# Kernel tuning notes

Hardware: AMD Instinct MI355X
Metric: run time of the kernel (lower is better)

Reference implementation:

```python
import jax, jax.numpy as jnp
import numpy as np

B = 192
D = 2048   # input_size
H = 128
LOG2PI = float(np.log(2.0 * np.pi))


def _linear_params(key, fan_in, fan_out):
    k1, k2 = jax.random.split(key)
    s = 1.0 / np.sqrt(fan_in)
    w = jax.random.uniform(k1, (fan_out, fan_in), minval=-s, maxval=s, dtype=jnp.float32)
    b = jax.random.uniform(k2, (fan_out,), minval=-s, maxval=s, dtype=jnp.float32)
    return w, b


def setup_inputs() -> dict:
    key = jax.random.key(0)
    ks = jax.random.split(key, 8)
    q = jax.random.normal(ks[0], (B, D), dtype=jnp.float32)
    eps = jax.random.normal(ks[1], (B, B, D), dtype=jnp.float32)  # rsample noise
    mu_w1, mu_b1 = _linear_params(ks[2], D, H)
    mu_w2, mu_b2 = _linear_params(ks[3], H, H)
    mu_w3, mu_b3 = _linear_params(ks[4], H, D)
    lv_w1, lv_b1 = _linear_params(ks[5], D, H)
    lv_w2, lv_b2 = _linear_params(ks[6], H, H)
    lv_w3, lv_b3 = _linear_params(ks[7], H, D)
    return dict(q=q, eps=eps,
                mu_w1=mu_w1, mu_b1=mu_b1, mu_w2=mu_w2, mu_b2=mu_b2, mu_w3=mu_w3, mu_b3=mu_b3,
                lv_w1=lv_w1, lv_b1=lv_b1, lv_w2=lv_w2, lv_b2=lv_b2, lv_w3=lv_w3, lv_b3=lv_b3)


def reference(q, eps, mu_w1, mu_b1, mu_w2, mu_b2, mu_w3, mu_b3,
              lv_w1, lv_b1, lv_w2, lv_b2, lv_w3, lv_b3):
    relu = jax.nn.relu
    # mu head (ReLU on every layer, including the last, as in the torch code)
    mu = relu(q @ mu_w1.T + mu_b1)
    mu = relu(mu @ mu_w2.T + mu_b2)
    mu = relu(mu @ mu_w3.T + mu_b3)                    # [B, D]
    # logvar head
    lv = relu(q @ lv_w1.T + lv_b1)
    lv = relu(lv @ lv_w2.T + lv_b2)
    lv = relu(lv @ lv_w3.T + lv_b3)                    # [B, D]
    # torch passes std_mat = diag(exp(0.5*logvar)) as COVARIANCE matrix,
    # so the diagonal variance is var = exp(0.5*logvar), per-dim scale = sqrt(var).
    var = jnp.exp(0.5 * lv)                            # [B, D] covariance diagonal
    scale = jnp.sqrt(var)                              # = exp(0.25*logvar)
    # rsample with sample_shape=(B,): p[i, j] = mu[j] + scale[j] * eps[i, j]
    p = mu[None, :, :] + eps * scale[None, :, :]       # [B, B, D]
    # diagonal-Gaussian log_prob of distribution j evaluated at p[i, j]
    diff = p - mu[None, :, :]
    maha = jnp.sum(diff * diff / var[None, :, :], axis=-1)       # [B, B]
    logdet = 0.5 * jnp.sum(lv, axis=-1)                          # sum(log var) = 0.5*sum(logvar)
    log_prob = -0.5 * (maha + D * LOG2PI) - 0.5 * logdet[None, :]  # [B, B]
    return p, log_prob
```

## Files before the change

kernel.cpp:

```cpp
#include <hip/hip_runtime.h>
#include <math.h>

#define BB 192
#define DD 2048
#define HH 128

#define D_LOG2PI 3763.9722320063395f

typedef float f32x4 __attribute__((ext_vector_type(4)));

__global__ __launch_bounds__(256) void head_kernel(
    const float* __restrict__ q,
    const float* __restrict__ mw1, const float* __restrict__ mb1,
    const float* __restrict__ mw2, const float* __restrict__ mb2,
    const float* __restrict__ mw3, const float* __restrict__ mb3,
    const float* __restrict__ lw1, const float* __restrict__ lb1,
    const float* __restrict__ lw2, const float* __restrict__ lb2,
    const float* __restrict__ lw3, const float* __restrict__ lb3,
    float* __restrict__ mu_out, float* __restrict__ scale_out,
    float* __restrict__ invvar_out, float* __restrict__ logdet_out)
{
    const int row  = blockIdx.x;
    const int head = blockIdx.y;
    const float* W1 = head ? lw1 : mw1;
    const float* B1 = head ? lb1 : mb1;
    const float* W2 = head ? lw2 : mw2;
    const float* B2 = head ? lb2 : mb2;
    const float* W3 = head ? lw3 : mw3;
    const float* B3 = head ? lb3 : mb3;

    __shared__ float qrow[DD];
    __shared__ float h1[HH];
    __shared__ float h2[HH];
    __shared__ float red[4];

    const int t = threadIdx.x;

    {
        const f32x4* src = (const f32x4*)(q + (size_t)row * DD);
        f32x4* dst = (f32x4*)qrow;
        for (int i = t; i < DD / 4; i += 256) dst[i] = src[i];
    }
    __syncthreads();

    {
        const int o = t >> 1, half = t & 1;
        const f32x4* w4 = (const f32x4*)(W1 + (size_t)o * DD + half * (DD / 2));
        const f32x4* x4 = (const f32x4*)(qrow + half * (DD / 2));
        float acc = 0.f;
        #pragma unroll 4
        for (int k = 0; k < DD / 8; ++k) {
            f32x4 w = w4[k], x = x4[k];
            acc += w.x * x.x + w.y * x.y + w.z * x.z + w.w * x.w;
        }
        acc += __shfl_xor(acc, 1);
        if (half == 0) h1[o] = fmaxf(acc + B1[o], 0.f);
    }
    __syncthreads();

    {
        const int o = t >> 1, half = t & 1;
        const f32x4* w4 = (const f32x4*)(W2 + o * HH + half * (HH / 2));
        const f32x4* x4 = (const f32x4*)(h1 + half * (HH / 2));
        float acc = 0.f;
        #pragma unroll
        for (int k = 0; k < HH / 8; ++k) {
            f32x4 w = w4[k], x = x4[k];
            acc += w.x * x.x + w.y * x.y + w.z * x.z + w.w * x.w;
        }
        acc += __shfl_xor(acc, 1);
        if (half == 0) h2[o] = fmaxf(acc + B2[o], 0.f);
    }
    __syncthreads();

    float sumlv = 0.f;
    for (int m = 0; m < DD / 256; ++m) {
        const int j = m * 256 + t;
        const f32x4* w4 = (const f32x4*)(W3 + (size_t)j * HH);
        const f32x4* x4 = (const f32x4*)h2;
        float acc = 0.f;
        #pragma unroll
        for (int k = 0; k < HH / 4; ++k) {
            f32x4 w = w4[k], x = x4[k];
            acc += w.x * x.x + w.y * x.y + w.z * x.z + w.w * x.w;
        }
        float val = fmaxf(acc + B3[j], 0.f);
        if (head == 0) {
            mu_out[(size_t)row * DD + j] = val;
        } else {
            float var = expf(0.5f * val);
            float sc  = sqrtf(var);
            scale_out [(size_t)row * DD + j] = sc;
            invvar_out[(size_t)row * DD + j] = 1.0f / var;
            sumlv += val;
        }
    }
    if (head == 1) {
        #pragma unroll
        for (int off = 32; off; off >>= 1) sumlv += __shfl_down(sumlv, off);
        const int wid = t >> 6, lane = t & 63;
        if (lane == 0) red[wid] = sumlv;
        __syncthreads();
        if (t == 0) logdet_out[row] = 0.5f * (red[0] + red[1] + red[2] + red[3]);
    }
}

__global__ __launch_bounds__(256) void sample_logprob_kernel(
    const float* __restrict__ eps,
    const float* __restrict__ mu, const float* __restrict__ scale,
    const float* __restrict__ invvar, const float* __restrict__ logdet,
    float* __restrict__ p_out, float* __restrict__ lp_out)
{
    const int i = blockIdx.x;
    const int j = blockIdx.y;
    const int t = threadIdx.x;

    const size_t base = ((size_t)(i * BB + j)) * DD;
    const f32x4* e4  = (const f32x4*)(eps + base);
    const f32x4* m4  = (const f32x4*)(mu + (size_t)j * DD);
    const f32x4* s4  = (const f32x4*)(scale + (size_t)j * DD);
    const f32x4* iv4 = (const f32x4*)(invvar + (size_t)j * DD);
    f32x4* p4 = (f32x4*)(p_out + base);

    float acc = 0.f;
    #pragma unroll
    for (int it = 0; it < DD / 1024; ++it) {
        const int idx = it * 256 + t;
        f32x4 e  = __builtin_nontemporal_load(&e4[idx]);
        f32x4 m  = m4[idx];
        f32x4 s  = s4[idx];
        f32x4 iv = iv4[idx];
        f32x4 pv;
        pv.x = m.x + e.x * s.x;
        pv.y = m.y + e.y * s.y;
        pv.z = m.z + e.z * s.z;
        pv.w = m.w + e.w * s.w;
        float dx = pv.x - m.x, dy = pv.y - m.y, dz = pv.z - m.z, dw = pv.w - m.w;
        acc += dx * dx * iv.x;
        acc += dy * dy * iv.y;
        acc += dz * dz * iv.z;
        acc += dw * dw * iv.w;
        __builtin_nontemporal_store(pv, &p4[idx]);
    }

    #pragma unroll
    for (int off = 32; off; off >>= 1) acc += __shfl_down(acc, off);
    __shared__ float red[4];
    const int wid = t >> 6, lane = t & 63;
    if (lane == 0) red[wid] = acc;
    __syncthreads();
    if (t == 0) {
        const float maha = red[0] + red[1] + red[2] + red[3];
        lp_out[(size_t)i * BB + j] = -0.5f * (maha + D_LOG2PI) - 0.5f * logdet[j];
    }
}

extern "C" void kernel_launch(void* const* d_in, const int* in_sizes, int n_in,
                              void* d_out, int out_size, void* d_ws, size_t ws_size,
                              hipStream_t stream) {
    (void)in_sizes; (void)n_in; (void)out_size; (void)ws_size;
    const float* q    = (const float*)d_in[0];
    const float* eps  = (const float*)d_in[1];
    const float* mw1  = (const float*)d_in[2];
    const float* mb1  = (const float*)d_in[3];
    const float* mw2  = (const float*)d_in[4];
    const float* mb2  = (const float*)d_in[5];
    const float* mw3  = (const float*)d_in[6];
    const float* mb3  = (const float*)d_in[7];
    const float* lw1  = (const float*)d_in[8];
    const float* lb1  = (const float*)d_in[9];
    const float* lw2  = (const float*)d_in[10];
    const float* lb2  = (const float*)d_in[11];
    const float* lw3  = (const float*)d_in[12];
    const float* lb3  = (const float*)d_in[13];

    float* ws      = (float*)d_ws;
    float* mu      = ws;
    float* scale   = ws + (size_t)BB * DD;
    float* invvar  = ws + 2 * (size_t)BB * DD;
    float* logdet  = ws + 3 * (size_t)BB * DD;

    float* p  = (float*)d_out;
    float* lp = p + (size_t)BB * BB * DD;

    head_kernel<<<dim3(BB, 2), 256, 0, stream>>>(
        q, mw1, mb1, mw2, mb2, mw3, mb3, lw1, lb1, lw2, lb2, lw3, lb3,
        mu, scale, invvar, logdet);

    sample_logprob_kernel<<<dim3(BB, BB), 256, 0, stream>>>(
        eps, mu, scale, invvar, logdet, p, lp);
}
```

Baseline: 656.2 us.

## Process two rows per head block with coalesced wave-level dot products; single-wave sample blocks

The head kernel now handles two batch rows per 512-thread block and reuses each weight load for both rows. Each layer is restructured so a wave (or half-wave) reads a weight row in a coalesced way and reduces with shuffles. The sample/log-prob kernel switches to 64-thread blocks, which removes the shared-memory reduction and block barrier. The intent is to halve weight traffic in the heads and cut per-block sync overhead in the bandwidth-bound sample kernel, at the cost of fewer, larger head blocks and more serial work per sample thread.

```diff
diff --git a/kernel.cpp b/kernel.cpp
--- a/kernel.cpp
+++ b/kernel.cpp
@@ -9,7 +9,7 @@
 
 typedef float f32x4 __attribute__((ext_vector_type(4)));
 
-__global__ __launch_bounds__(256) void head_kernel(
+__global__ __launch_bounds__(512) void head_kernel(
     const float* __restrict__ q,
     const float* __restrict__ mw1, const float* __restrict__ mb1,
     const float* __restrict__ mw2, const float* __restrict__ mb2,
@@ -20,7 +20,7 @@
     float* __restrict__ mu_out, float* __restrict__ scale_out,
     float* __restrict__ invvar_out, float* __restrict__ logdet_out)
 {
-    const int row  = blockIdx.x;
+    const int row0 = blockIdx.x * 2;
     const int head = blockIdx.y;
     const float* W1 = head ? lw1 : mw1;
     const float* B1 = head ? lb1 : mb1;
@@ -29,83 +29,138 @@
     const float* W3 = head ? lw3 : mw3;
     const float* B3 = head ? lb3 : mb3;
 
-    __shared__ float qrow[DD];
-    __shared__ float h1[HH];
-    __shared__ float h2[HH];
-    __shared__ float red[4];
-
-    const int t = threadIdx.x;
-
-    {
-        const f32x4* src = (const f32x4*)(q + (size_t)row * DD);
+    __shared__ float qrow[2 * DD];
+    __shared__ float h1[2][HH];
+    __shared__ float h2[2][HH];
+    __shared__ float red[8][2];
+
+    const int t    = threadIdx.x;
+    const int wave = t >> 6;
+    const int lane = t & 63;
+    const int half = lane >> 5;
+    const int kl   = lane & 31;
+
+    {
+        const f32x4* src = (const f32x4*)(q + (size_t)row0 * DD);
         f32x4* dst = (f32x4*)qrow;
-        for (int i = t; i < DD / 4; i += 256) dst[i] = src[i];
+        #pragma unroll
+        for (int it = 0; it < (2 * DD / 4) / 512; ++it)
+            dst[it * 512 + t] = src[it * 512 + t];
     }
     __syncthreads();
 
     {
-        const int o = t >> 1, half = t & 1;
-        const f32x4* w4 = (const f32x4*)(W1 + (size_t)o * DD + half * (DD / 2));
-        const f32x4* x4 = (const f32x4*)(qrow + half * (DD / 2));
-        float acc = 0.f;
-        #pragma unroll 4
-        for (int k = 0; k < DD / 8; ++k) {
-            f32x4 w = w4[k], x = x4[k];
-            acc += w.x * x.x + w.y * x.y + w.z * x.z + w.w * x.w;
-        }
-        acc += __shfl_xor(acc, 1);
-        if (half == 0) h1[o] = fmaxf(acc + B1[o], 0.f);
+        const f32x4* q0 = (const f32x4*)qrow;
+        const f32x4* q1 = (const f32x4*)(qrow + DD);
+        for (int oi = 0; oi < 16; ++oi) {
+            const int o = wave * 16 + oi;
+            const f32x4* w4 = (const f32x4*)(W1 + (size_t)o * DD);
+            float a0 = 0.f, a1 = 0.f;
+            #pragma unroll
+            for (int k = 0; k < DD / 4 / 64; ++k) {
+                f32x4 w  = w4[k * 64 + lane];
+                f32x4 x0 = q0[k * 64 + lane];
+                f32x4 x1 = q1[k * 64 + lane];
+                a0 += w.x * x0.x + w.y * x0.y + w.z * x0.z + w.w * x0.w;
+                a1 += w.x * x1.x + w.y * x1.y + w.z * x1.z + w.w * x1.w;
+            }
+            #pragma unroll
+            for (int off = 32; off; off >>= 1) {
+                a0 += __shfl_xor(a0, off);
+                a1 += __shfl_xor(a1, off);
+            }
+            if (lane == 0) {
+                const float b = B1[o];
+                h1[0][o] = fmaxf(a0 + b, 0.f);
+                h1[1][o] = fmaxf(a1 + b, 0.f);
+            }
+        }
     }
     __syncthreads();
 
     {
-        const int o = t >> 1, half = t & 1;
-        const f32x4* w4 = (const f32x4*)(W2 + o * HH + half * (HH / 2));
-        const f32x4* x4 = (const f32x4*)(h1 + half * (HH / 2));
-        float acc = 0.f;
+        const f32x4* x0 = (const f32x4*)h1[0];
+        const f32x4* x1 = (const f32x4*)h1[1];
         #pragma unroll
-        for (int k = 0; k < HH / 8; ++k) {
-            f32x4 w = w4[k], x = x4[k];
-            acc += w.x * x.x + w.y * x.y + w.z * x.z + w.w * x.w;
-        }
-        acc += __shfl_xor(acc, 1);
-        if (half == 0) h2[o] = fmaxf(acc + B2[o], 0.f);
+        for (int pi = 0; pi < 8; ++pi) {
+            const int o = wave * 16 + pi * 2 + half;
+            const f32x4* w4 = (const f32x4*)(W2 + (size_t)o * HH);
+            f32x4 w  = w4[kl];
+            f32x4 v0 = x0[kl];
+            f32x4 v1 = x1[kl];
+            float a0 = w.x * v0.x + w.y * v0.y + w.z * v0.z + w.w * v0.w;
+            float a1 = w.x * v1.x + w.y * v1.y + w.z * v1.z + w.w * v1.w;
+            #pragma unroll
+            for (int off = 16; off; off >>= 1) {
+                a0 += __shfl_xor(a0, off);
+                a1 += __shfl_xor(a1, off);
+            }
+            if (kl == 0) {
+                const float b = B2[o];
+                h2[0][o] = fmaxf(a0 + b, 0.f);
+                h2[1][o] = fmaxf(a1 + b, 0.f);
+            }
+        }
     }
     __syncthreads();
 
-    float sumlv = 0.f;
-    for (int m = 0; m < DD / 256; ++m) {
-        const int j = m * 256 + t;
-        const f32x4* w4 = (const f32x4*)(W3 + (size_t)j * HH);
-        const f32x4* x4 = (const f32x4*)h2;
-        float acc = 0.f;
-        #pragma unroll
-        for (int k = 0; k < HH / 4; ++k) {
-            f32x4 w = w4[k], x = x4[k];
-            acc += w.x * x.x + w.y * x.y + w.z * x.z + w.w * x.w;
-        }
-        float val = fmaxf(acc + B3[j], 0.f);
-        if (head == 0) {
-            mu_out[(size_t)row * DD + j] = val;
-        } else {
-            float var = expf(0.5f * val);
-            float sc  = sqrtf(var);
-            scale_out [(size_t)row * DD + j] = sc;
-            invvar_out[(size_t)row * DD + j] = 1.0f / var;
-            sumlv += val;
-        }
-    }
+    float slv0 = 0.f, slv1 = 0.f;
+    {
+        const f32x4* x0 = (const f32x4*)h2[0];
+        const f32x4* x1 = (const f32x4*)h2[1];
+        for (int pi = 0; pi < 128; ++pi) {
+            const int o = wave * 256 + pi * 2 + half;
+            const f32x4* w4 = (const f32x4*)(W3 + (size_t)o * HH);
+            f32x4 w  = w4[kl];
+            f32x4 v0 = x0[kl];
+            f32x4 v1 = x1[kl];
+            float a0 = w.x * v0.x + w.y * v0.y + w.z * v0.z + w.w * v0.w;
+            float a1 = w.x * v1.x + w.y * v1.y + w.z * v1.z + w.w * v1.w;
+            #pragma unroll
+            for (int off = 16; off; off >>= 1) {
+                a0 += __shfl_xor(a0, off);
+                a1 += __shfl_xor(a1, off);
+            }
+            if (kl == 0) {
+                const float b = B3[o];
+                const float r0 = fmaxf(a0 + b, 0.f);
+                const float r1 = fmaxf(a1 + b, 0.f);
+                if (head == 0) {
+                    mu_out[(size_t)row0 * DD + o]       = r0;
+                    mu_out[(size_t)(row0 + 1) * DD + o] = r1;
+                } else {
+                    const float var0 = expf(0.5f * r0);
+                    const float var1 = expf(0.5f * r1);
+                    scale_out [(size_t)row0 * DD + o]       = sqrtf(var0);
+                    scale_out [(size_t)(row0 + 1) * DD + o] = sqrtf(var1);
+                    invvar_out[(size_t)row0 * DD + o]       = 1.0f / var0;
+                    invvar_out[(size_t)(row0 + 1) * DD + o] = 1.0f / var1;
+                    slv0 += r0;
+                    slv1 += r1;
+                }
+            }
+        }
+    }
+
     if (head == 1) {
         #pragma unroll
-        for (int off = 32; off; off >>= 1) sumlv += __shfl_down(sumlv, off);
-        const int wid = t >> 6, lane = t & 63;
-        if (lane == 0) red[wid] = sumlv;
+        for (int off = 32; off; off >>= 1) {
+            slv0 += __shfl_down(slv0, off);
+            slv1 += __shfl_down(slv1, off);
+        }
+        if (lane == 0) { red[wave][0] = slv0; red[wave][1] = slv1; }
         __syncthreads();
-        if (t == 0) logdet_out[row] = 0.5f * (red[0] + red[1] + red[2] + red[3]);
+        if (t == 0) {
+            float s0 = 0.f, s1 = 0.f;
+            #pragma unroll
+            for (int w = 0; w < 8; ++w) { s0 += red[w][0]; s1 += red[w][1]; }
+            logdet_out[row0]     = 0.5f * s0;
+            logdet_out[row0 + 1] = 0.5f * s1;
+        }
     }
 }
 
-__global__ __launch_bounds__(256) void sample_logprob_kernel(
+__global__ __launch_bounds__(64) void sample_logprob_kernel(
     const float* __restrict__ eps,
     const float* __restrict__ mu, const float* __restrict__ scale,
     const float* __restrict__ invvar, const float* __restrict__ logdet,
@@ -123,9 +178,9 @@
     f32x4* p4 = (f32x4*)(p_out + base);
 
     float acc = 0.f;
-    #pragma unroll
-    for (int it = 0; it < DD / 1024; ++it) {
-        const int idx = it * 256 + t;
+    #pragma unroll 4
+    for (int it = 0; it < DD / 256; ++it) {
+        const int idx = it * 64 + t;
         f32x4 e  = __builtin_nontemporal_load(&e4[idx]);
         f32x4 m  = m4[idx];
         f32x4 s  = s4[idx];
@@ -135,7 +190,7 @@
         pv.y = m.y + e.y * s.y;
         pv.z = m.z + e.z * s.z;
         pv.w = m.w + e.w * s.w;
-        float dx = pv.x - m.x, dy = pv.y - m.y, dz = pv.z - m.z, dw = pv.w - m.w;
+        const float dx = pv.x - m.x, dy = pv.y - m.y, dz = pv.z - m.z, dw = pv.w - m.w;
         acc += dx * dx * iv.x;
         acc += dy * dy * iv.y;
         acc += dz * dz * iv.z;
@@ -145,14 +200,8 @@
 
     #pragma unroll
     for (int off = 32; off; off >>= 1) acc += __shfl_down(acc, off);
-    __shared__ float red[4];
-    const int wid = t >> 6, lane = t & 63;
-    if (lane == 0) red[wid] = acc;
-    __syncthreads();
-    if (t == 0) {
-        const float maha = red[0] + red[1] + red[2] + red[3];
-        lp_out[(size_t)i * BB + j] = -0.5f * (maha + D_LOG2PI) - 0.5f * logdet[j];
-    }
+    if (t == 0)
+        lp_out[(size_t)i * BB + j] = -0.5f * (acc + D_LOG2PI) - 0.5f * logdet[j];
 }
 
 extern "C" void kernel_launch(void* const* d_in, const int* in_sizes, int n_in,
@@ -174,19 +223,19 @@
     const float* lw3  = (const float*)d_in[12];
     const float* lb3  = (const float*)d_in[13];
 
-    float* ws      = (float*)d_ws;
-    float* mu      = ws;
-    float* scale   = ws + (size_t)BB * DD;
-    float* invvar  = ws + 2 * (size_t)BB * DD;
-    float* logdet  = ws + 3 * (size_t)BB * DD;
+    float* ws     = (float*)d_ws;
+    float* mu     = ws;
+    float* scale  = ws + (size_t)BB * DD;
+    float* invvar = ws + 2 * (size_t)BB * DD;
+    float* logdet = ws + 3 * (size_t)BB * DD;
 
     float* p  = (float*)d_out;
     float* lp = p + (size_t)BB * BB * DD;
 
-    head_kernel<<<dim3(BB, 2), 256, 0, stream>>>(
+    head_kernel<<<dim3(BB / 2, 2), 512, 0, stream>>>(
         q, mw1, mb1, mw2, mb2, mw3, mb3, lw1, lb1, lw2, lb2, lw3, lb3,
         mu, scale, invvar, logdet);
 
-    sample_logprob_kernel<<<dim3(BB, BB), 256, 0, stream>>>(
+    sample_logprob_kernel<<<dim3(BB, BB), 64, 0, stream>>>(
         eps, mu, scale, invvar, logdet, p, lp);
 }
```

Measured after the change: 674.2 us. 1.03x slower.
